# Kernel tuning notes

Hardware: AMD Instinct MI355X
Metric: run time of the kernel (lower is better)

## Reference

```python
import jax, jax.numpy as jnp
import numpy as np

B, T, C, H = 256, 256, 384, 6
HS = C // H        # 64 head size
P = int(C * 0.8)   # 307 pca_dim
EPS = 1e-6


def _rmsnorm(x, scale):
    rms = jnp.sqrt(jnp.mean(x * x, axis=-1, keepdims=True) + EPS)
    return x / rms * scale


def _orth(W):
    # torch.svd returns V (not V^T); u @ v.t() == u @ vt
    u, _, vt = jnp.linalg.svd(W, full_matrices=False)
    return u @ vt


def setup_inputs() -> dict:
    key = jax.random.key(0)
    ks = jax.random.split(key, 16)
    s = 0.02
    inp = {
        'x': jax.random.normal(ks[0], (B, T, C), jnp.float32),
        'Wq': jax.random.normal(ks[1], (H, C, HS), jnp.float32) * s,
        'Wk': jax.random.normal(ks[2], (H, C, HS), jnp.float32) * s,
        'Wv': jax.random.normal(ks[3], (H, C, HS), jnp.float32) * s,
        'Wp': jax.random.normal(ks[4], (H * HS, C), jnp.float32) * s,
        'bp': jnp.zeros((C,), jnp.float32),
        'scale1': jnp.ones((C,), jnp.float32),
        'scale2': jnp.ones((C,), jnp.float32),
        'W1': jax.random.normal(ks[5], (C, P), jnp.float32) * s,
        'b1': jnp.zeros((P,), jnp.float32),
        'W2': jax.random.normal(ks[6], (P, C), jnp.float32) * s,
        'b2': jnp.zeros((C,), jnp.float32),
        'Wo_in': jax.random.normal(ks[7], (C, C), jnp.float32),
        'Wo_out': jax.random.normal(ks[8], (C, C), jnp.float32),
    }
    return inp


def reference(x, Wq, Wk, Wv, Wp, bp, scale1, scale2, W1, b1, W2, b2, Wo_in, Wo_out):
    # ln1
    h = _rmsnorm(x, scale1)                                   # [B,T,C]
    # multi-head causal self-attention (heads batched via einsum)
    q = jnp.einsum('btc,hcd->bhtd', h, Wq)                    # [B,H,T,HS]
    k = jnp.einsum('btc,hcd->bhtd', h, Wk)
    v = jnp.einsum('btc,hcd->bhtd', h, Wv)
    wei = jnp.einsum('bhtd,bhsd->bhts', q, k) * (HS ** -0.5)  # [B,H,T,T]
    causal = jnp.tril(jnp.ones((T, T), bool))
    wei = jnp.where(causal, wei, -jnp.inf)
    wei = jax.nn.softmax(wei, axis=-1)
    attn = jnp.einsum('bhts,bhsd->bhtd', wei, v)              # [B,H,T,HS]
    attn = attn.transpose(0, 2, 1, 3).reshape(B, T, H * HS)   # concat heads
    h = attn @ Wp + bp + h                                    # residual on ln1 output
    # ln2
    h = _rmsnorm(h, scale2)
    # input orthogonal transform
    h = h @ _orth(Wo_in)
    # PCA feed-forward (dropout = identity in eval)
    h = jax.nn.relu(h @ W1 + b1)
    h = h @ W2 + b2
    # output orthogonal transform + residual on ff output
    out = h @ _orth(Wo_out) + h
    return out
```

## Files before the change

kernel.cpp:

```cpp
#include <hip/hip_runtime.h>

typedef unsigned short u16;
typedef unsigned int   u32;
typedef short s16x8 __attribute__((ext_vector_type(8)));
typedef float f32x4 __attribute__((ext_vector_type(4)));

static __device__ __forceinline__ float bf2f(u16 v){ return __uint_as_float(((u32)v)<<16); }
static __device__ __forceinline__ u16 f2bf(float f){
  u32 u = __float_as_uint(f);
  u32 r = (u + 0x7fffu + ((u>>16)&1u)) >> 16;
  return (u16)r;
}
static __device__ __forceinline__ float cvt(float v){ return v; }
static __device__ __forceinline__ float cvt(u16 v){ return bf2f(v); }
static __device__ __forceinline__ void stv(float* p, float v){ *p = v; }
static __device__ __forceinline__ void stv(u16* p, float v){ *p = f2bf(v); }

static __device__ __forceinline__ void ld2(const float* p, float& a, float& b){
  float2 t = *(const float2*)p; a=t.x; b=t.y;
}
static __device__ __forceinline__ void ld2(const u16* p, float& a, float& b){
  u32 t = *(const u32*)p; a = __uint_as_float(t<<16); b = __uint_as_float(t & 0xffff0000u);
}
static __device__ __forceinline__ void st2(float* p, float a, float b){
  float2 t; t.x=a; t.y=b; *(float2*)p = t;
}
static __device__ __forceinline__ void st2(u16* p, float a, float b){
  *(u32*)p = ((u32)f2bf(a)) | (((u32)f2bf(b))<<16);
}

template<typename TI, typename TO>
__global__ __launch_bounds__(256) void rms_k(const TI* __restrict__ X,
                                             const float* __restrict__ scale,
                                             TO* __restrict__ O)
{
  int row = blockIdx.x*4 + (threadIdx.x>>6);
  int lane = threadIdx.x&63;
  const TI* xr = X + (size_t)row*384;
  float v[6]; float ss = 0.f;
#pragma unroll
  for(int i=0;i<3;i++){
    ld2(xr + 2*lane + 128*i, v[2*i], v[2*i+1]);
    ss += v[2*i]*v[2*i] + v[2*i+1]*v[2*i+1];
  }
#pragma unroll
  for(int off=32; off>0; off>>=1) ss += __shfl_down(ss, off, 64);
  ss = __shfl(ss, 0, 64);
  float r = rsqrtf(ss*(1.0f/384.0f)+1e-6f);
  TO* orow = O + (size_t)row*384;
#pragma unroll
  for(int i=0;i<3;i++){
    int c = 2*lane + 128*i;
    st2(orow + c, v[2*i]*r*scale[c], v[2*i+1]*r*scale[c+1]);
  }
}

__global__ __launch_bounds__(256) void tcast_k(const float* __restrict__ In, long isz,
                                               u16* __restrict__ Out, long osz,
                                               int Rr, int Cc, int ldo)
{
  __shared__ float t[32][33];
  const int z = blockIdx.z;
  const float* I = In + (long)z*isz;
  u16* Oz = Out + (long)z*osz;
  const int r0 = blockIdx.x*32, c0 = blockIdx.y*32;
  const int tx = threadIdx.x&31, ty = threadIdx.x>>5;
#pragma unroll
  for(int rr=ty; rr<32; rr+=8){
    int r = r0+rr, c = c0+tx;
    t[rr][tx] = (r<Rr && c<Cc) ? I[(size_t)r*Cc + c] : 0.f;
  }
  __syncthreads();
#pragma unroll
  for(int cc=ty; cc<32; cc+=8){
    int c = c0+cc, r = r0+tx;
    if(c<Cc && r<ldo) Oz[(size_t)c*ldo + r] = f2bf(t[tx][cc]);
  }
}

template<typename TC, typename TR>
__global__ __launch_bounds__(256,4) void mgemm_k(
    const u16* __restrict__ A, int lda, long asz,
    const u16* __restrict__ Bt, int ldb, long bsz,
    TC* __restrict__ C, long csz, long cs_hi, int cs_lo,
    const TR* __restrict__ R, long rsz,
    const float* __restrict__ bias,
    int M, int N, int Nstore, int K, float beta, int relu)
{
  __shared__ __align__(16) u16 As[128*40];
  __shared__ __align__(16) u16 Bs[64*40];
  const int z = blockIdx.z;
  const u16* Az = A + (long)z*asz;
  const u16* Bz = Bt + (long)z*bsz;
  const int m0 = blockIdx.x*128, n0 = blockIdx.y*64;
  const int tid = threadIdx.x;
  const int w = tid>>6, lane = tid&63;
  const int g4 = lane>>4, l16 = lane&15;
  const int wr = w>>1, wc = w&1;
  const int arow = tid>>2, akc = (tid&3)*8;

  const u16* gA0 = Az + (size_t)(m0+arow)*lda + akc;
  const u16* gA1 = Az + (size_t)(m0+64+arow)*lda + akc;
  const bool bok = (n0 + arow) < N;
  const u16* gB  = Bz + (size_t)(bok ? (n0+arow) : 0)*ldb + akc;
  uint4* dA0 = (uint4*)&As[arow*40 + akc];
  uint4* dA1 = (uint4*)&As[(64+arow)*40 + akc];
  uint4* dB  = (uint4*)&Bs[arow*40 + akc];
  if(!bok){ *dB = make_uint4(0,0,0,0); }

  f32x4 fz = {0.f,0.f,0.f,0.f};
  f32x4 acc[4][2];
#pragma unroll
  for(int i=0;i<4;i++)
#pragma unroll
    for(int j=0;j<2;j++) acc[i][j]=fz;

  for(int k0=0;k0<K;k0+=32){
    *dA0 = *(const uint4*)gA0;  gA0 += 32;
    *dA1 = *(const uint4*)gA1;  gA1 += 32;
    if(bok){ *dB = *(const uint4*)gB; gB += 32; }
    __syncthreads();
    s16x8 av[4], bv[2];
#pragma unroll
    for(int mf=0;mf<4;mf++)
      av[mf] = *(const s16x8*)&As[(wr*64 + mf*16 + l16)*40 + g4*8];
#pragma unroll
    for(int nf=0;nf<2;nf++)
      bv[nf] = *(const s16x8*)&Bs[(wc*32 + nf*16 + l16)*40 + g4*8];
#pragma unroll
    for(int mf=0;mf<4;mf++)
#pragma unroll
      for(int nf=0;nf<2;nf++)
        acc[mf][nf] = __builtin_amdgcn_mfma_f32_16x16x32_bf16(av[mf], bv[nf], acc[mf][nf], 0,0,0);
    __syncthreads();
  }
#pragma unroll
  for(int mf=0;mf<4;mf++)
#pragma unroll
    for(int i=0;i<4;i++){
      int m = m0 + wr*64 + mf*16 + g4*4 + i;
      long rowoff = (long)(m>>8)*cs_hi + (long)(m&255)*cs_lo;
#pragma unroll
      for(int nf=0;nf<2;nf++){
        int n = n0 + wc*32 + nf*16 + l16;
        if(n < Nstore){
          float v = 0.f;
          if(n < N){
            v = acc[mf][nf][i];
            if(R)    v += beta*cvt(R[rowoff + (long)z*rsz + n]);
            if(bias) v += bias[n];
            if(relu) v  = fmaxf(v, 0.f);
          }
          stv(C + (long)z*csz + rowoff + n, v);
        }
      }
    }
}

__global__ __launch_bounds__(256,2) void mattn_k(const u16* __restrict__ QKV,
                                                 u16* __restrict__ O)
{
  __shared__ __align__(16) u16 Ks[64*64];
  __shared__ __align__(16) u16 Vts[64*64];
  __shared__ __align__(16) u16 Ps[4*4096];
  const int bh = blockIdx.x;
  const int b = bh/6, h = bh - b*6;
  const u16* Qb = QKV + (size_t)bh*49152;
  const u16* Kb = Qb + 16384;
  const u16* Vb = Qb + 32768;
  const int tid = threadIdx.x;
  const int w = tid>>6, lane = tid&63;
  const int g4 = lane>>4, l16 = lane&15;
  char* PB = (char*)&Ps[w*4096];
  const int swz = (l16&7)<<4;

  s16x8 qf[4][2];
#pragma unroll
  for(int mi=0;mi<4;mi++)
#pragma unroll
    for(int ks=0;ks<2;ks++)
      qf[mi][ks] = *(const s16x8*)(Qb + (size_t)(w*64 + mi*16 + l16)*64 + ks*32 + g4*8);

  f32x4 fzv = {0.f,0.f,0.f,0.f};
  f32x4 o[4][4];
#pragma unroll
  for(int mf=0;mf<4;mf++)
#pragma unroll
    for(int df=0;df<4;df++) o[mf][df]=fzv;
  float mrun[4], lrun[4];
#pragma unroll
  for(int mi=0;mi<4;mi++){ mrun[mi]=-1e30f; lrun[mi]=0.f; }

  for(int st=0; st<4; ++st){
    if(st) __syncthreads();
#pragma unroll
    for(int it=0; it<2; ++it){
      int c = tid + 256*it;
      int s = c>>3, d0 = (c&7)*8;
      uint4 ld = *(const uint4*)(Kb + (size_t)(st*64+s)*64 + d0);
      int byte = s*128 + d0*2; byte ^= (s&7)<<4;
      *(uint4*)((char*)Ks + byte) = ld;
    }
#pragma unroll
    for(int it=0; it<2; ++it){
      int c = tid + 256*it;
      int s = c&63, d0 = (c>>6)*8;
      uint4 ld = *(const uint4*)(Vb + (size_t)(st*64+s)*64 + d0);
#pragma unroll
      for(int jj=0; jj<4; ++jj){
        u32 ww = (jj==0)?ld.x:(jj==1)?ld.y:(jj==2)?ld.z:ld.w;
        int d = d0 + 2*jj;
        int byte0 = d*128 + s*2;     byte0 ^= (d&7)<<4;
        int byte1 = (d+1)*128 + s*2; byte1 ^= ((d+1)&7)<<4;
        *(u16*)((char*)Vts + byte0) = (u16)(ww & 0xffffu);
        *(u16*)((char*)Vts + byte1) = (u16)(ww >> 16);
      }
    }
    __syncthreads();
    if(w < st) continue;

    f32x4 sc[4][4];
#pragma unroll
    for(int sf=0; sf<4; ++sf){
      int row = sf*16 + l16;
      s16x8 kf0 = *(const s16x8*)((char*)Ks + ((row*128 + g4*16) ^ swz));
      s16x8 kf1 = *(const s16x8*)((char*)Ks + ((row*128 + 64 + g4*16) ^ swz));
#pragma unroll
      for(int mi=0; mi<4; ++mi){
        f32x4 t = __builtin_amdgcn_mfma_f32_16x16x32_bf16(kf0, qf[mi][0], fzv, 0,0,0);
        sc[sf][mi] = __builtin_amdgcn_mfma_f32_16x16x32_bf16(kf1, qf[mi][1], t, 0,0,0);
      }
    }
    float alpha[4];
#pragma unroll
    for(int mi=0; mi<4; ++mi){
      int mloc = mi*16 + l16;
      float rmax = -3.0e38f;
#pragma unroll
      for(int sf=0; sf<4; ++sf)
#pragma unroll
        for(int i=0;i<4;i++){
          float vv = sc[sf][mi][i]*0.125f;
          if(st==w && (sf*16 + g4*4 + i) > mloc) vv = -1e30f;
          sc[sf][mi][i] = vv;
          rmax = fmaxf(rmax, vv);
        }
      rmax = fmaxf(rmax, __shfl_xor(rmax, 16, 64));
      rmax = fmaxf(rmax, __shfl_xor(rmax, 32, 64));
      float mnew = fmaxf(mrun[mi], rmax);
      float al = __expf(mrun[mi] - mnew);
      mrun[mi] = mnew;
      float ls = 0.f;
#pragma unroll
      for(int sf=0; sf<4; ++sf){
        float p0 = __expf(sc[sf][mi][0]-mnew);
        float p1 = __expf(sc[sf][mi][1]-mnew);
        float p2 = __expf(sc[sf][mi][2]-mnew);
        float p3 = __expf(sc[sf][mi][3]-mnew);
        ls += p0+p1+p2+p3;
        ushort4 pk; pk.x=f2bf(p0); pk.y=f2bf(p1); pk.z=f2bf(p2); pk.w=f2bf(p3);
        int byte = mloc*128 + sf*32 + g4*8; byte ^= (l16&7)<<4;
        *(ushort4*)(PB + byte) = pk;
      }
      ls += __shfl_xor(ls, 16, 64);
      ls += __shfl_xor(ls, 32, 64);
      lrun[mi] = lrun[mi]*al + ls;
      alpha[mi] = al;
    }
#pragma unroll
    for(int mf=0; mf<4; ++mf)
#pragma unroll
      for(int i=0;i<4;i++){
        float at = __shfl(alpha[mf], g4*4 + i, 64);
#pragma unroll
        for(int df=0; df<4; ++df) o[mf][df][i] *= at;
      }
    s16x8 vbf[4][2];
#pragma unroll
    for(int df=0; df<4; ++df){
      int row = df*16 + l16;
      vbf[df][0] = *(const s16x8*)((char*)Vts + ((row*128 + g4*16) ^ swz));
      vbf[df][1] = *(const s16x8*)((char*)Vts + ((row*128 + 64 + g4*16) ^ swz));
    }
#pragma unroll
    for(int mf=0; mf<4; ++mf){
      int row = mf*16 + l16;
      s16x8 pa0 = *(const s16x8*)(PB + ((row*128 + g4*16) ^ swz));
      s16x8 pa1 = *(const s16x8*)(PB + ((row*128 + 64 + g4*16) ^ swz));
#pragma unroll
      for(int df=0; df<4; ++df){
        f32x4 t = __builtin_amdgcn_mfma_f32_16x16x32_bf16(pa0, vbf[df][0], o[mf][df], 0,0,0);
        o[mf][df] = __builtin_amdgcn_mfma_f32_16x16x32_bf16(pa1, vbf[df][1], t, 0,0,0);
      }
    }
  }
#pragma unroll
  for(int mf=0; mf<4; ++mf)
#pragma unroll
    for(int i=0;i<4;i++){
      float lt = __shfl(lrun[mf], g4*4 + i, 64);
      float rl = 1.f/lt;
      u16* orow = O + ((size_t)(b*256 + w*64 + mf*16 + g4*4 + i))*384 + h*64;
#pragma unroll
      for(int df=0; df<4; ++df)
        orow[df*16 + l16] = f2bf(o[mf][df][i]*rl);
    }
}


__global__ __launch_bounds__(256) void fpart_k(const float* __restrict__ W0,
                                               const float* __restrict__ W1,
                                               float* __restrict__ part)
{
  int b = blockIdx.x; int z = b/24, seg = b - z*24;
  const float* W = (z ? W1 : W0) + seg*6144;
  int tid = threadIdx.x;
  float s = 0.f;
  for(int i=tid;i<6144;i+=256){ float v=W[i]; s+=v*v; }
#pragma unroll
  for(int off=32; off>0; off>>=1) s += __shfl_down(s, off, 64);
  __shared__ float red[4];
  if((tid&63)==0) red[tid>>6]=s;
  __syncthreads();
  if(tid==0) part[b] = red[0]+red[1]+red[2]+red[3];
}

__global__ __launch_bounds__(64) void fcomb_k(const float* __restrict__ part,
                                              float* __restrict__ invb)
{
  int lane = threadIdx.x;
  float v = 0.f;
  if(lane < 24) v = part[lane];
  else if(lane >= 32 && lane < 56) v = part[lane - 8];
#pragma unroll
  for(int off=1; off<32; off<<=1) v += __shfl_xor(v, off, 64);
  if(lane==0)  invb[0] = rsqrtf(v);
  if(lane==32) invb[1] = rsqrtf(v);
}

__global__ __launch_bounds__(256) void nsinit_k(const float* __restrict__ W0,
                                                const float* __restrict__ W1,
                                                const float* __restrict__ invb,
                                                u16* __restrict__ XB)
{
  int b = blockIdx.x; int z = b/24, p = b - z*24, cp0 = p*16;
  const float* W = z ? W1 : W0;
  float inv = invb[z];
  u16* base = XB + (size_t)z*589824;
  u16* xh = base;            u16* xl = base + 147456;
  u16* th = base + 294912;   u16* tl = base + 442368;
  int tid = threadIdx.x;
  for(int idx=tid; idx<6144; idx+=256){
    int r = idx>>4, j = idx&15;
    float v = W[r*384 + cp0 + j]*inv;
    u16 hh = f2bf(v);
    xh[p*6144 + idx] = hh;
    xl[p*6144 + idx] = f2bf(v - bf2f(hh));
  }
  for(int idx=tid; idx<6144; idx+=256){
    int j = idx/384, r = idx - j*384;
    float v = W[(cp0+j)*384 + r]*inv;
    u16 hh = f2bf(v);
    th[p*6144 + r*16 + j] = hh;
    tl[p*6144 + r*16 + j] = f2bf(v - bf2f(hh));
  }
}

static __device__ __forceinline__ void ns_mm(
    const u16* __restrict__ Agh, const u16* __restrict__ Agl,
    u16* AhL, u16* AlL, const u16* BThL, const u16* BTlL,
    int tid, f32x4 acc[4])
{
  const int w = tid>>6, lane = tid&63, g4 = lane>>4, l16 = lane&15;
  const int o0 = (tid>>1)*24 + (tid&1)*8;
  const int o1 = o0 + 4608;
  const s16x8 z8 = {0,0,0,0,0,0,0,0};
  f32x4 fz = {0.f,0.f,0.f,0.f};
#pragma unroll
  for(int i=0;i<4;i++) acc[i]=fz;
  {
    uint4 h0 = *(const uint4*)(Agh + tid*8);
    uint4 h1 = *(const uint4*)(Agh + (384+tid)*8);
    uint4 l0 = *(const uint4*)(Agl + tid*8);
    uint4 l1 = *(const uint4*)(Agl + (384+tid)*8);
    *(uint4*)&AhL[o0] = h0; *(uint4*)&AhL[o1] = h1;
    *(uint4*)&AlL[o0] = l0; *(uint4*)&AlL[o1] = l1;
  }
  __syncthreads();
  for(int c=0;c<24;c++){
    uint4 nh0, nh1, nl0, nl1;
    if(c<23){
      const u16* ph = Agh + (c+1)*6144;
      const u16* pl = Agl + (c+1)*6144;
      nh0 = *(const uint4*)(ph + tid*8);
      nh1 = *(const uint4*)(ph + (384+tid)*8);
      nl0 = *(const uint4*)(pl + tid*8);
      nl1 = *(const uint4*)(pl + (384+tid)*8);
    }
    s16x8 bh = z8, bl = z8;
    if(g4<2){
      bh = *(const s16x8*)&BThL[l16*392 + c*16 + g4*8];
      bl = *(const s16x8*)&BTlL[l16*392 + c*16 + g4*8];
    }
#pragma unroll
    for(int tt=0;tt<4;tt++){
      int rb = 64*w + 16*tt + l16;
      s16x8 ah = z8, al = z8;
      if(g4<2){
        ah = *(const s16x8*)&AhL[rb*24 + g4*8];
        al = *(const s16x8*)&AlL[rb*24 + g4*8];
      }
      acc[tt] = __builtin_amdgcn_mfma_f32_16x16x32_bf16(ah, bh, acc[tt], 0,0,0);
      acc[tt] = __builtin_amdgcn_mfma_f32_16x16x32_bf16(ah, bl, acc[tt], 0,0,0);
      acc[tt] = __builtin_amdgcn_mfma_f32_16x16x32_bf16(al, bh, acc[tt], 0,0,0);
    }
    __syncthreads();
    if(c<23){
      *(uint4*)&AhL[o0] = nh0; *(uint4*)&AhL[o1] = nh1;
      *(uint4*)&AlL[o0] = nl0; *(uint4*)&AlL[o1] = nl1;
      __syncthreads();
    }
  }
}

__global__ __launch_bounds__(384) void nsit_k(u16* __restrict__ XB,
                                              u16* __restrict__ QT,
                                              int it, int niter, int nq)
{
  __shared__ __align__(16) u16 AhL[384*24];
  __shared__ __align__(16) u16 AlL[384*24];
  __shared__ __align__(16) u16 BTh[16*392];
  __shared__ __align__(16) u16 BTl[16*392];
  const int blk = blockIdx.x;
  const int z = blk/24, p = blk - z*24, cp0 = p*16;
  const int tid = threadIdx.x;
  const int w = tid>>6, lane = tid&63, g4 = lane>>4, l16 = lane&15;
  const int rs = it&1, ws2 = rs^1;
  const u16* bin  = XB + (size_t)rs*1179648  + (size_t)z*589824;
  u16*       bout = XB + (size_t)ws2*1179648 + (size_t)z*589824;
  const u16* Xh  = bin;            const u16* Xl  = bin + 147456;
  const u16* Th  = bin + 294912;   const u16* Tl  = bin + 442368;

  {
    const u16* sh = Xh + p*6144;
    const u16* sl = Xl + p*6144;
    for(int i=tid; i<768; i+=384){
      int k = i>>1, n0 = (i&1)*8;
      uint4 vh = *(const uint4*)(sh + i*8);
      uint4 vl = *(const uint4*)(sl + i*8);
#pragma unroll
      for(int j=0;j<8;j++){
        BTh[(n0+j)*392 + k] = ((u16*)&vh)[j];
        BTl[(n0+j)*392 + k] = ((u16*)&vl)[j];
      }
    }
  }
  __syncthreads();

  const bool quint = (it < nq);
  f32x4 acc[4], gsv[4];

  ns_mm(Th, Tl, AhL, AlL, BTh, BTl, tid, acc);
  if(quint){
#pragma unroll
    for(int tt=0;tt<4;tt++){
      gsv[tt] = acc[tt];
      int m0 = 64*w + 16*tt + g4*4;
      ushort4 h4, l4;
#pragma unroll
      for(int i=0;i<4;i++){
        float v = acc[tt][i];
        u16 hh = f2bf(v);
        ((u16*)&h4)[i]=hh; ((u16*)&l4)[i]=f2bf(v - bf2f(hh));
      }
      *(ushort4*)&BTh[l16*392 + m0] = h4;
      *(ushort4*)&BTl[l16*392 + m0] = l4;
    }
    __syncthreads();
    ns_mm(Xh, Xl, AhL, AlL, BTh, BTl, tid, acc);
#pragma unroll
    for(int tt=0;tt<4;tt++){
      int m0 = 64*w + 16*tt + g4*4;
      ushort4 h4, l4;
#pragma unroll
      for(int i=0;i<4;i++){
        float v = acc[tt][i];
        u16 hh = f2bf(v);
        ((u16*)&h4)[i]=hh; ((u16*)&l4)[i]=f2bf(v - bf2f(hh));
      }
      *(ushort4*)&BTh[l16*392 + m0] = h4;
      *(ushort4*)&BTl[l16*392 + m0] = l4;
    }
    __syncthreads();
    ns_mm(Th, Tl, AhL, AlL, BTh, BTl, tid, acc);
#pragma unroll
    for(int tt=0;tt<4;tt++){
      int m0 = 64*w + 16*tt + g4*4;
      ushort4 h4, l4;
#pragma unroll
      for(int i=0;i<4;i++){
        float v = fmaf(2.0315f, acc[tt][i], -4.7750f*gsv[tt][i])
                + ((m0+i)==(cp0+l16) ? 3.4445f : 0.f);
        u16 hh = f2bf(v);
        ((u16*)&h4)[i]=hh; ((u16*)&l4)[i]=f2bf(v - bf2f(hh));
      }
      *(ushort4*)&BTh[l16*392 + m0] = h4;
      *(ushort4*)&BTl[l16*392 + m0] = l4;
    }
    __syncthreads();
  } else {
#pragma unroll
    for(int tt=0;tt<4;tt++){
      int m0 = 64*w + 16*tt + g4*4;
      ushort4 h4, l4;
#pragma unroll
      for(int i=0;i<4;i++){
        float v = -0.5f*acc[tt][i] + ((m0+i)==(cp0+l16) ? 1.5f : 0.f);
        u16 hh = f2bf(v);
        ((u16*)&h4)[i]=hh; ((u16*)&l4)[i]=f2bf(v - bf2f(hh));
      }
      *(ushort4*)&BTh[l16*392 + m0] = h4;
      *(ushort4*)&BTl[l16*392 + m0] = l4;
    }
    __syncthreads();
  }
  ns_mm(Xh, Xl, AhL, AlL, BTh, BTl, tid, acc);

  if(it == niter-1){
    u16* q = QT + (size_t)z*147456 + (size_t)(cp0+l16)*384;
#pragma unroll
    for(int tt=0;tt<4;tt++){
      int m0 = 64*w + 16*tt + g4*4;
      ushort4 h4;
#pragma unroll
      for(int i=0;i<4;i++) ((u16*)&h4)[i] = f2bf(acc[tt][i]);
      *(ushort4*)&q[m0] = h4;
    }
  } else {
    u16* oXh = bout + p*6144;            u16* oXl = bout + 147456 + p*6144;
    u16* oTh = bout + 294912;            u16* oTl = bout + 442368;
#pragma unroll
    for(int tt=0;tt<4;tt++){
      int m0 = 64*w + 16*tt + g4*4;
      ushort4 h4, l4;
#pragma unroll
      for(int i=0;i<4;i++){
        float v = acc[tt][i];
        u16 hh = f2bf(v);
        ((u16*)&h4)[i]=hh; ((u16*)&l4)[i]=f2bf(v - bf2f(hh));
        oXh[(m0+i)*16 + l16] = hh;
        oXl[(m0+i)*16 + l16] = ((u16*)&l4)[i];
      }
      size_t to = (size_t)(4*w+tt)*6144 + (size_t)(cp0+l16)*16 + g4*4;
      *(ushort4*)&oTh[to] = h4;
      *(ushort4*)&oTl[to] = l4;
    }
  }
}

extern "C" void kernel_launch(void* const* d_in, const int* in_sizes, int n_in,
                              void* d_out, int out_size, void* d_ws, size_t ws_size,
                              hipStream_t stream)
{
  const float* x      = (const float*)d_in[0];
  const float* Wq     = (const float*)d_in[1];
  const float* Wk     = (const float*)d_in[2];
  const float* Wv     = (const float*)d_in[3];
  const float* Wp     = (const float*)d_in[4];
  const float* bp     = (const float*)d_in[5];
  const float* scale1 = (const float*)d_in[6];
  const float* scale2 = (const float*)d_in[7];
  const float* W1     = (const float*)d_in[8];
  const float* b1     = (const float*)d_in[9];
  const float* W2     = (const float*)d_in[10];
  const float* b2     = (const float*)d_in[11];
  const float* Wo_in  = (const float*)d_in[12];
  const float* Wo_out = (const float*)d_in[13];

  char* ws = (char*)d_ws;
  u16* XB   = (u16*)(ws + 0);
  u16* Wqkv = (u16*)(ws + 4719104L);
  u16* WpT  = (u16*)(ws + 5603840L);
  u16* W1T  = (u16*)(ws + 5898752L);
  u16* W2T  = (u16*)(ws + 6134528L);
  u16* QT   = (u16*)(ws + 6380288L);
  float* part = (float*)(ws + 6970112L);
  float* invb = (float*)(ws + 6970496L);
  u16* h1b  = (u16*)(ws + 8388608L);
  u16* qkvb = (u16*)(ws + 58720256L);
  u16* atb  = (u16*)(ws + 209715200L);
  u16* h2b = qkvb;
  u16* h3b = qkvb + 25165824L;
  u16* h4b = qkvb + 50331648L;
  u16* h5b = atb;
  u16* h6b = h1b;

  tcast_k<<<dim3(12, 2,6),256,0,stream>>>(Wq,24576L, Wqkv,        73728L, 384, 64,384);
  tcast_k<<<dim3(12, 2,6),256,0,stream>>>(Wk,24576L, Wqkv+24576L, 73728L, 384, 64,384);
  tcast_k<<<dim3(12, 2,6),256,0,stream>>>(Wv,24576L, Wqkv+49152L, 73728L, 384, 64,384);
  tcast_k<<<dim3(12,12,1),256,0,stream>>>(Wp,0L,     WpT,0L,     384,384,384);
  tcast_k<<<dim3(12,10,1),256,0,stream>>>(W1,0L,     W1T,0L,     384,307,384);
  tcast_k<<<dim3(10,12,1),256,0,stream>>>(W2,0L,     W2T,0L,     307,384,320);

  const int NITER = 15, NQ = 10;
  fpart_k<<<48,256,0,stream>>>(Wo_in, Wo_out, part);
  fcomb_k<<<1,64,0,stream>>>(part, invb);
  nsinit_k<<<48,256,0,stream>>>(Wo_in, Wo_out, invb, XB);
  for(int it=0; it<NITER; ++it)
    nsit_k<<<48,384,0,stream>>>(XB, QT, it, NITER, NQ);

  rms_k<float,u16><<<16384,256,0,stream>>>(x, scale1, h1b);
  mgemm_k<u16,float><<<dim3(512,1,18),256,0,stream>>>(
      h1b,384,0L,  Wqkv,384,24576L,
      qkvb,16384L,294912L,64,  (const float*)nullptr,0L, nullptr,
      65536,64,64,384, 0.f,0);
  mattn_k<<<1536,256,0,stream>>>(qkvb, atb);
  mgemm_k<u16,u16><<<dim3(512,6,1),256,0,stream>>>(
      atb,384,0L,  WpT,384,0L,
      h2b,0L,98304L,384,  h1b,0L, bp,
      65536,384,384,384, 1.f,0);
  rms_k<u16,u16><<<16384,256,0,stream>>>(h2b, scale2, h3b);
  mgemm_k<u16,float><<<dim3(512,6,1),256,0,stream>>>(
      h3b,384,0L,  QT,384,0L,
      h4b,0L,98304L,384,  (const float*)nullptr,0L, nullptr,
      65536,384,384,384, 0.f,0);
  mgemm_k<u16,float><<<dim3(512,5,1),256,0,stream>>>(
      h4b,384,0L,  W1T,384,0L,
      h5b,0L,81920L,320,  (const float*)nullptr,0L, b1,
      65536,307,320,384, 0.f,1);
  mgemm_k<u16,float><<<dim3(512,6,1),256,0,stream>>>(
      h5b,320,0L,  W2T,320,0L,
      h6b,0L,98304L,384,  (const float*)nullptr,0L, b2,
      65536,384,384,320, 0.f,0);
  mgemm_k<float,u16><<<dim3(512,6,1),256,0,stream>>>(
      h6b,384,0L,  QT+147456,384,0L,
      (float*)d_out,0L,98304L,384,  h6b,0L, nullptr,
      65536,384,384,384, 1.f,0);

  (void)in_sizes; (void)n_in; (void)ws_size; (void)out_size;
}
```

Baseline: 1.595 ms.

## Widen GEMM N-tiles to full rows and map blocks per XCD

```diff
diff --git a/kernel.cpp b/kernel.cpp
--- a/kernel.cpp
+++ b/kernel.cpp
@@ -78,60 +78,71 @@
   }
 }
 
-template<typename TC, typename TR>
-__global__ __launch_bounds__(256,4) void mgemm_k(
-    const u16* __restrict__ A, int lda, long asz,
-    const u16* __restrict__ Bt, int ldb, long bsz,
-    TC* __restrict__ C, long csz, long cs_hi, int cs_lo,
-    const TR* __restrict__ R, long rsz,
+template<int NF, typename TC, typename TR>
+__global__ __launch_bounds__(256,2) void mgemmN_k(
+    const u16* __restrict__ A, int lda,
+    const u16* __restrict__ Bt, int ldb,
+    TC* __restrict__ C, long cs_hi, int cs_lo, int csz,
+    const TR* __restrict__ R,
     const float* __restrict__ bias,
-    int M, int N, int Nstore, int K, float beta, int relu)
-{
+    int N, int Nstore, int K, float beta, int relu, int nby)
+{
+  constexpr int BN = NF*32;
   __shared__ __align__(16) u16 As[128*40];
-  __shared__ __align__(16) u16 Bs[64*40];
-  const int z = blockIdx.z;
-  const u16* Az = A + (long)z*asz;
-  const u16* Bz = Bt + (long)z*bsz;
-  const int m0 = blockIdx.x*128, n0 = blockIdx.y*64;
+  __shared__ __align__(16) u16 Bs[BN*40];
+  const int d = blockIdx.x;
+  const int xcd = d&7, slot = d>>3;
+  const int bm = xcd*64 + slot/nby;
+  const int bn = slot - (slot/nby)*nby;
+  const int m0 = bm*128, n0 = bn*BN;
   const int tid = threadIdx.x;
   const int w = tid>>6, lane = tid&63;
   const int g4 = lane>>4, l16 = lane&15;
   const int wr = w>>1, wc = w&1;
-  const int arow = tid>>2, akc = (tid&3)*8;
-
-  const u16* gA0 = Az + (size_t)(m0+arow)*lda + akc;
-  const u16* gA1 = Az + (size_t)(m0+64+arow)*lda + akc;
-  const bool bok = (n0 + arow) < N;
-  const u16* gB  = Bz + (size_t)(bok ? (n0+arow) : 0)*ldb + akc;
-  uint4* dA0 = (uint4*)&As[arow*40 + akc];
-  uint4* dA1 = (uint4*)&As[(64+arow)*40 + akc];
-  uint4* dB  = (uint4*)&Bs[arow*40 + akc];
-  if(!bok){ *dB = make_uint4(0,0,0,0); }
+  const int arow = tid>>1, akc = (tid&1)*16;
 
   f32x4 fz = {0.f,0.f,0.f,0.f};
-  f32x4 acc[4][2];
+  f32x4 acc[4][NF];
 #pragma unroll
   for(int i=0;i<4;i++)
 #pragma unroll
-    for(int j=0;j<2;j++) acc[i][j]=fz;
+    for(int j=0;j<NF;j++) acc[i][j]=fz;
 
   for(int k0=0;k0<K;k0+=32){
-    *dA0 = *(const uint4*)gA0;  gA0 += 32;
-    *dA1 = *(const uint4*)gA1;  gA1 += 32;
-    if(bok){ *dB = *(const uint4*)gB; gB += 32; }
-    __syncthreads();
-    s16x8 av[4], bv[2];
+    {
+      const u16* ga = &A[(size_t)(m0+arow)*lda + k0 + akc];
+      uint4 a0 = *(const uint4*)ga;
+      uint4 a1 = *(const uint4*)(ga+8);
+      *(uint4*)&As[arow*40 + akc]     = a0;
+      *(uint4*)&As[arow*40 + akc + 8] = a1;
+    }
+#pragma unroll
+    for(int j=0;j<(BN+127)/128;j++){
+      int brow = (tid>>1) + 128*j;
+      if(brow < BN){
+        int gn = n0 + brow;
+        uint4 b0 = make_uint4(0,0,0,0), b1 = b0;
+        if(gn < N){
+          const u16* gb = &Bt[(size_t)gn*ldb + k0 + akc];
+          b0 = *(const uint4*)gb;
+          b1 = *(const uint4*)(gb+8);
+        }
+        *(uint4*)&Bs[brow*40 + akc]     = b0;
+        *(uint4*)&Bs[brow*40 + akc + 8] = b1;
+      }
+    }
+    __syncthreads();
+    s16x8 av[4];
 #pragma unroll
     for(int mf=0;mf<4;mf++)
       av[mf] = *(const s16x8*)&As[(wr*64 + mf*16 + l16)*40 + g4*8];
 #pragma unroll
-    for(int nf=0;nf<2;nf++)
-      bv[nf] = *(const s16x8*)&Bs[(wc*32 + nf*16 + l16)*40 + g4*8];
-#pragma unroll
-    for(int mf=0;mf<4;mf++)
-#pragma unroll
-      for(int nf=0;nf<2;nf++)
-        acc[mf][nf] = __builtin_amdgcn_mfma_f32_16x16x32_bf16(av[mf], bv[nf], acc[mf][nf], 0,0,0);
+    for(int nf=0;nf<NF;nf++){
+      s16x8 bv = *(const s16x8*)&Bs[(wc*(NF*16) + nf*16 + l16)*40 + g4*8];
+#pragma unroll
+      for(int mf=0;mf<4;mf++)
+        acc[mf][nf] = __builtin_amdgcn_mfma_f32_16x16x32_bf16(av[mf], bv, acc[mf][nf], 0,0,0);
+    }
     __syncthreads();
   }
 #pragma unroll
@@ -141,17 +152,18 @@
       int m = m0 + wr*64 + mf*16 + g4*4 + i;
       long rowoff = (long)(m>>8)*cs_hi + (long)(m&255)*cs_lo;
 #pragma unroll
-      for(int nf=0;nf<2;nf++){
-        int n = n0 + wc*32 + nf*16 + l16;
-        if(n < Nstore){
+      for(int nf=0;nf<NF;nf++){
+        int gn = n0 + wc*(NF*16) + nf*16 + l16;
+        if(gn < Nstore){
+          long addr = rowoff + (long)(gn>>6)*csz + (gn&63);
           float v = 0.f;
-          if(n < N){
+          if(gn < N){
             v = acc[mf][nf][i];
-            if(R)    v += beta*cvt(R[rowoff + (long)z*rsz + n]);
-            if(bias) v += bias[n];
+            if(R)    v += beta*cvt(R[addr]);
+            if(bias) v += bias[gn];
             if(relu) v  = fmaxf(v, 0.f);
           }
-          stv(C + (long)z*csz + rowoff + n, v);
+          stv(C + addr, v);
         }
       }
     }
@@ -307,7 +319,6 @@
     }
 }
 
-
 __global__ __launch_bounds__(256) void fpart_k(const float* __restrict__ W0,
                                                const float* __restrict__ W1,
                                                float* __restrict__ part)
@@ -493,13 +504,17 @@
     }
     __syncthreads();
     ns_mm(Th, Tl, AhL, AlL, BTh, BTl, tid, acc);
+    __syncthreads();
 #pragma unroll
     for(int tt=0;tt<4;tt++){
       int m0 = 64*w + 16*tt + g4*4;
+      ushort4 gh = *(const ushort4*)&BTh[l16*392 + m0];
+      ushort4 gl = *(const ushort4*)&BTl[l16*392 + m0];
+      (void)gh; (void)gl;
       ushort4 h4, l4;
 #pragma unroll
       for(int i=0;i<4;i++){
-        float v = fmaf(2.0315f, acc[tt][i], -4.7750f*gsv[tt][i])
+        float v = fmaf(2.0315f, acc[tt][i], -4.7750f*(gsv[tt][i]))
                 + ((m0+i)==(cp0+l16) ? 3.4445f : 0.f);
         u16 hh = f2bf(v);
         ((u16*)&h4)[i]=hh; ((u16*)&l4)[i]=f2bf(v - bf2f(hh));
@@ -610,32 +625,38 @@
     nsit_k<<<48,384,0,stream>>>(XB, QT, it, NITER, NQ);
 
   rms_k<float,u16><<<16384,256,0,stream>>>(x, scale1, h1b);
-  mgemm_k<u16,float><<<dim3(512,1,18),256,0,stream>>>(
-      h1b,384,0L,  Wqkv,384,24576L,
-      qkvb,16384L,294912L,64,  (const float*)nullptr,0L, nullptr,
-      65536,64,64,384, 0.f,0);
+  mgemmN_k<12,u16,float><<<1536,256,0,stream>>>(
+      h1b,384,  Wqkv,384,
+      qkvb, 294912L,64,16384,
+      (const float*)nullptr, nullptr,
+      1152,1152,384, 0.f,0, 3);
   mattn_k<<<1536,256,0,stream>>>(qkvb, atb);
-  mgemm_k<u16,u16><<<dim3(512,6,1),256,0,stream>>>(
-      atb,384,0L,  WpT,384,0L,
-      h2b,0L,98304L,384,  h1b,0L, bp,
-      65536,384,384,384, 1.f,0);
+  mgemmN_k<12,u16,u16><<<512,256,0,stream>>>(
+      atb,384,  WpT,384,
+      h2b, 98304L,384,64,
+      h1b, bp,
+      384,384,384, 1.f,0, 1);
   rms_k<u16,u16><<<16384,256,0,stream>>>(h2b, scale2, h3b);
-  mgemm_k<u16,float><<<dim3(512,6,1),256,0,stream>>>(
-      h3b,384,0L,  QT,384,0L,
-      h4b,0L,98304L,384,  (const float*)nullptr,0L, nullptr,
-      65536,384,384,384, 0.f,0);
-  mgemm_k<u16,float><<<dim3(512,5,1),256,0,stream>>>(
-      h4b,384,0L,  W1T,384,0L,
-      h5b,0L,81920L,320,  (const float*)nullptr,0L, b1,
-      65536,307,320,384, 0.f,1);
-  mgemm_k<u16,float><<<dim3(512,6,1),256,0,stream>>>(
-      h5b,320,0L,  W2T,320,0L,
-      h6b,0L,98304L,384,  (const float*)nullptr,0L, b2,
-      65536,384,384,320, 0.f,0);
-  mgemm_k<float,u16><<<dim3(512,6,1),256,0,stream>>>(
-      h6b,384,0L,  QT+147456,384,0L,
-      (float*)d_out,0L,98304L,384,  h6b,0L, nullptr,
-      65536,384,384,384, 1.f,0);
+  mgemmN_k<12,u16,float><<<512,256,0,stream>>>(
+      h3b,384,  QT,384,
+      h4b, 98304L,384,64,
+      (const float*)nullptr, nullptr,
+      384,384,384, 0.f,0, 1);
+  mgemmN_k<10,u16,float><<<512,256,0,stream>>>(
+      h4b,384,  W1T,384,
+      h5b, 81920L,320,64,
+      (const float*)nullptr, b1,
+      307,320,384, 0.f,1, 1);
+  mgemmN_k<12,u16,float><<<512,256,0,stream>>>(
+      h5b,320,  W2T,320,
+      h6b, 98304L,384,64,
+      (const float*)nullptr, b2,
+      384,384,320, 0.f,0, 1);
+  mgemmN_k<12,float,u16><<<512,256,0,stream>>>(
+      h6b,384,  QT+147456,384,
+      (float*)d_out, 98304L,384,64,
+      h6b, nullptr,
+      384,384,384, 1.f,0, 1);
 
   (void)in_sizes; (void)n_in; (void)ws_size; (void)out_size;
 }
```

Measured after the change: 1.700 ms. +6.6%, slower.
